# Performance work log

Measured on AMD Instinct MI355X. Metric: run time of the kernel, lower is better.

The kernel has to match this reference:

```python
import jax, jax.numpy as jnp
import numpy as np

N_NODES = 50000
N_EDGES = 800000
IN_CH = 128
EDGE_DIM = 32
H1, H2, H3, OUT = 128, 64, 32, 1


def _linear_params(key, fan_in, fan_out, bias=True):
    k1, k2 = jax.random.split(key)
    scale = 1.0 / np.sqrt(fan_in)
    W = jax.random.uniform(k1, (fan_in, fan_out), jnp.float32, -scale, scale)
    if bias:
        b = jax.random.uniform(k2, (fan_out,), jnp.float32, -scale, scale)
        return W, b
    return W


def setup_inputs() -> dict:
    key = jax.random.key(0)
    ks = jax.random.split(key, 32)
    inp = {
        'x': jax.random.normal(ks[0], (N_NODES, IN_CH), jnp.float32),
        'edge_index': jax.random.randint(ks[1], (2, N_EDGES), 0, N_NODES, jnp.int64),
        'edge_attr': jax.random.normal(ks[2], (N_EDGES, EDGE_DIM), jnp.float32),
    }
    dims = [(IN_CH, H1), (H1, H2), (H2, H3)]
    ki = 3
    for l, (fi, fo) in enumerate(dims, start=1):
        inp[f'Wq{l}'], inp[f'bq{l}'] = _linear_params(ks[ki], fi, fo); ki += 1
        inp[f'Wk{l}'], inp[f'bk{l}'] = _linear_params(ks[ki], fi, fo); ki += 1
        inp[f'Wv{l}'], inp[f'bv{l}'] = _linear_params(ks[ki], fi, fo); ki += 1
        inp[f'We{l}'] = _linear_params(ks[ki], EDGE_DIM, fo, bias=False); ki += 1
        inp[f'Ws{l}'], inp[f'bs{l}'] = _linear_params(ks[ki], fi, fo); ki += 1
    inp['Wc'], inp['bc'] = _linear_params(ks[ki], H3, OUT)
    return inp


def _tconv(x, src, dst, edge_attr, Wq, bq, Wk, bk, Wv, bv, We, Ws, bs):
    # TransformerConv, heads=1: edge-conditioned attention with segment softmax over dst
    q = x @ Wq + bq                      # [N, d]
    k = x @ Wk + bk                      # [N, d]
    v = x @ Wv + bv                      # [N, d]
    e = edge_attr @ We                   # [E, d]
    k_e = k[src] + e                     # gather + edge key
    v_e = v[src] + e                     # gather + edge value
    d = q.shape[-1]
    alpha = jnp.sum(q[dst] * k_e, axis=-1) / jnp.sqrt(jnp.asarray(d, x.dtype))  # [E]
    m = jax.ops.segment_max(alpha, dst, num_segments=N_NODES)
    a = jnp.exp(alpha - m[dst])
    s = jax.ops.segment_sum(a, dst, num_segments=N_NODES)
    a = a / s[dst]
    agg = jax.ops.segment_sum(a[:, None] * v_e, dst, num_segments=N_NODES)
    return agg + x @ Ws + bs             # root/skip connection


def reference(x, edge_index, edge_attr,
              Wq1, bq1, Wk1, bk1, Wv1, bv1, We1, Ws1, bs1,
              Wq2, bq2, Wk2, bk2, Wv2, bv2, We2, Ws2, bs2,
              Wq3, bq3, Wk3, bk3, Wv3, bv3, We3, Ws3, bs3,
              Wc, bc):
    src, dst = edge_index[0], edge_index[1]
    h = jax.nn.relu(_tconv(x, src, dst, edge_attr, Wq1, bq1, Wk1, bk1, Wv1, bv1, We1, Ws1, bs1))
    h = jax.nn.relu(_tconv(h, src, dst, edge_attr, Wq2, bq2, Wk2, bk2, Wv2, bv2, We2, Ws2, bs2))
    h = jax.nn.relu(_tconv(h, src, dst, edge_attr, Wq3, bq3, Wk3, bk3, Wv3, bv3, We3, Ws3, bs3))
    return h @ Wc + bc
```

## Files before the change

### kernel.cpp

```cpp
#include <hip/hip_runtime.h>
#include <math.h>

#define N_NODES 50000
#define N_EDGES 800000

typedef __bf16 bf16;
typedef __bf16 bf16x8 __attribute__((ext_vector_type(8)));
typedef float f32x4 __attribute__((ext_vector_type(4)));

__device__ __forceinline__ float bflo(unsigned r) {
  union { unsigned u; float f; } c; c.u = r << 16; return c.f;
}
__device__ __forceinline__ float bfhi(unsigned r) {
  union { unsigned u; float f; } c; c.u = r & 0xffff0000u; return c.f;
}

__device__ __forceinline__ float dot2bf(unsigned a, unsigned b, float acc) {
#if defined(__has_builtin)
#if __has_builtin(__builtin_amdgcn_fdot2_f32_bf16)
  typedef __bf16 bf16x2 __attribute__((ext_vector_type(2)));
  union { unsigned u; bf16x2 v; } ca, cb;
  ca.u = a; cb.u = b;
  return __builtin_amdgcn_fdot2_f32_bf16(ca.v, cb.v, acc, false);
#else
  return acc + bflo(a) * bflo(b) + bfhi(a) * bfhi(b);
#endif
#else
  return acc + bflo(a) * bflo(b) + bfhi(a) * bfhi(b);
#endif
}

__global__ void k_detect(const int* ei, int* flags) {
  if (threadIdx.x == 0 && blockIdx.x == 0) {
    int is64 = 1;
    for (int i = 0; i < 128; ++i) {
      if (ei[2 * i + 1] != 0) { is64 = 0; break; }
    }
    flags[0] = is64;
  }
}

__device__ __forceinline__ int load_idx(const int* ei, int e, int is64, int which) {
  size_t idx = (size_t)which * N_EDGES + (size_t)e;
  return is64 ? ei[2 * idx] : ei[idx];
}


__global__ void k_zero(int* p, int n) {
  int i = blockIdx.x * blockDim.x + threadIdx.x;
  if (i < n) p[i] = 0;
}

__global__ void k_hist(const int* ei, const int* flags, int* counts) {
  int e = blockIdx.x * blockDim.x + threadIdx.x;
  int is64 = flags[0];
  if (e < N_EDGES) {
    int dst = load_idx(ei, e, is64, 1);
    if (dst >= 0 && dst < N_NODES) atomicAdd(&counts[dst], 1);
  }
}

__global__ void k_scan1(const int* counts, int* row_ptr, int* bsum) {
  __shared__ int buf[1024];
  int t = threadIdx.x;
  int i = blockIdx.x * 1024 + t;
  int v = (i < N_NODES) ? counts[i] : 0;
  buf[t] = v;
  __syncthreads();
  for (int off = 1; off < 1024; off <<= 1) {
    int x = (t >= off) ? buf[t - off] : 0;
    __syncthreads();
    buf[t] += x;
    __syncthreads();
  }
  if (i < N_NODES) row_ptr[i] = buf[t] - v;
  if (t == 1023) bsum[blockIdx.x] = buf[1023];
}

__global__ void k_scan2(int* bsum, int* row_ptr) {
  constexpr int NB = (N_NODES + 1023) / 1024;
  int t = threadIdx.x;
  int v = (t < NB) ? bsum[t] : 0;
  int inc = v;
#pragma unroll
  for (int off = 1; off < 64; off <<= 1) {
    int x = __shfl_up(inc, off, 64);
    if (t >= off) inc += x;
  }
  if (t < NB) bsum[t] = inc - v;
  if (t == 63) row_ptr[N_NODES] = inc;
}

__global__ void k_scan3(const int* bsum, int* row_ptr, int* cursor) {
  int i = blockIdx.x * 1024 + threadIdx.x;
  if (i < N_NODES) {
    int r = row_ptr[i] + bsum[blockIdx.x];
    row_ptr[i] = r;
    cursor[i] = r;
  }
}

__global__ void k_scatter(const int* ei, const int* flags, int* cursor,
                          int* csr_src, int* csr_eid) {
  int e = blockIdx.x * blockDim.x + threadIdx.x;
  int is64 = flags[0];
  if (e < N_EDGES) {
    int src = load_idx(ei, e, is64, 0);
    int dst = load_idx(ei, e, is64, 1);
    if (dst >= 0 && dst < N_NODES && src >= 0 && src < N_NODES) {
      int pos = atomicAdd(&cursor[dst], 1);
      if (pos >= 0 && pos < N_EDGES) {
        csr_src[pos] = src;
        csr_eid[pos] = e;
      }
    }
  }
}


__global__ void k_eaperm(const float* __restrict__ ea, const int* __restrict__ csr_eid,
                         bf16* __restrict__ ea_bf) {
  int idx = blockIdx.x * blockDim.x + threadIdx.x;
  if (idx >= N_EDGES * 16) return;
  int p = idx >> 4, jj = idx & 15;
  int eid = csr_eid[p];
  float2 t = *(const float2*)(ea + (size_t)eid * 32 + 2 * jj);
  union { bf16 b[2]; unsigned u; } c;
  c.b[0] = (bf16)t.x; c.b[1] = (bf16)t.y;
  *(unsigned*)(ea_bf + (size_t)p * 32 + 2 * jj) = c.u;
}


#define DBLK 256
#define NDB ((N_NODES + DBLK - 1) / DBLK)

__global__ void k_dhist(const int* __restrict__ counts, int* __restrict__ btot) {
  __shared__ int lh[64];
  int t = threadIdx.x;
  if (t < 64) lh[t] = 0;
  __syncthreads();
  int n = blockIdx.x * DBLK + t;
  if (n < N_NODES) atomicAdd(&lh[min(counts[n], 63)], 1);
  __syncthreads();
  if (t < 64 && lh[t] > 0) atomicAdd(&btot[t], lh[t]);
}

__global__ void k_dbase(const int* __restrict__ btot, int* __restrict__ dcursor) {
  int t = threadIdx.x;
  int v = btot[t];
  int inc = v;
#pragma unroll
  for (int off = 1; off < 64; off <<= 1) {
    int x = __shfl_up(inc, off, 64);
    if (t >= off) inc += x;
  }
  dcursor[t] = inc - v;
}

__global__ void k_dscatter(const int* __restrict__ counts, int* __restrict__ dcursor,
                           int* __restrict__ node_perm) {
  __shared__ int lh[64];
  __shared__ int lbase[64];
  int t = threadIdx.x;
  if (t < 64) lh[t] = 0;
  __syncthreads();
  int n = blockIdx.x * DBLK + t;
  int b = 0, lrank = 0;
  bool valid = (n < N_NODES);
  if (valid) {
    b = min(counts[n], 63);
    lrank = atomicAdd(&lh[b], 1);
  }
  __syncthreads();
  if (t < 64) {
    int c = lh[t];
    lbase[t] = (c > 0) ? atomicAdd(&dcursor[t], c) : 0;
  }
  __syncthreads();
  if (valid) node_perm[lbase[b] + lrank] = n;
}


template <int FI, int FO>
__global__ void k_prep(const float* __restrict__ Wq, const float* __restrict__ bq,
                       const float* __restrict__ Wk, const float* __restrict__ bk,
                       const float* __restrict__ Wv, const float* __restrict__ bv,
                       const float* __restrict__ We,
                       const float* __restrict__ Ws, const float* __restrict__ bs,
                       bf16* __restrict__ Wt, float* __restrict__ bias) {
  constexpr int CPL = FO / 16;
  int n = blockIdx.x;
  int k = threadIdx.x;
  int pos;
  if (n < 4 * FO) {
    int sel = n / FO, c = n - sel * FO;
    if (sel == 0) pos = c;
    else if (sel == 3) pos = 3 * FO + c;
    else {
      int g = c / CPL, o = c - g * CPL;
      pos = FO + g * 2 * CPL + (sel == 2 ? CPL : 0) + o;
    }
  } else {
    pos = n;
  }
  if (n < 4 * FO) {
    int sel = n / FO, c = n - sel * FO;
    const float* W = sel == 0 ? Wq : sel == 1 ? Wk : sel == 2 ? Wv : Ws;
    Wt[(size_t)pos * FI + k] = (bf16)W[(size_t)k * FO + c];
    if (k == 0) bias[pos] = (sel == 0 ? bq : sel == 1 ? bk : sel == 2 ? bv : bs)[c];
  } else {
    int j = n - 4 * FO;
    float acc = 0.f;
    for (int c = 0; c < FO; ++c) acc += Wq[(size_t)k * FO + c] * We[(size_t)j * FO + c];
    Wt[(size_t)pos * FI + k] = (bf16)acc;
    if (k == 0) {
      float b = 0.f;
      for (int c = 0; c < FO; ++c) b += bq[c] * We[(size_t)j * FO + c];
      bias[pos] = b;
    }
  }
}


template <int K, int NT, bool AF32>
__global__ __launch_bounds__(256) void k_gemm_mfma(const void* __restrict__ A,
                                                   const bf16* __restrict__ Wt,
                                                   const float* __restrict__ bias,
                                                   bf16* __restrict__ feat) {
  constexpr int NKB = K / 32;
  constexpr int NCH = (NT + 63) / 64;
  int lane = threadIdx.x & 63;
  int wave = threadIdx.x >> 6;
  int m0 = blockIdx.x * 64 + wave * 16;
  if (m0 >= N_NODES) return;
  int half = lane & 15;
  int quad = lane >> 4;

  bf16x8 afr[NKB];
#pragma unroll
  for (int kb = 0; kb < NKB; ++kb) {
    size_t aoff = (size_t)(m0 + half) * K + kb * 32 + quad * 8;
    if constexpr (AF32) {
      const float* Af = (const float*)A;
      f32x4 lo = *(const f32x4*)(Af + aoff);
      f32x4 hi = *(const f32x4*)(Af + aoff + 4);
#pragma unroll
      for (int j = 0; j < 4; ++j) { afr[kb][j] = (bf16)lo[j]; afr[kb][4 + j] = (bf16)hi[j]; }
    } else {
      afr[kb] = *(const bf16x8*)((const bf16*)A + aoff);
    }
  }

  for (int ch = 0; ch < NCH; ++ch) {
    int c0 = ch * 64;
    f32x4 acc[4] = {};
#pragma unroll
    for (int kb = 0; kb < NKB; ++kb) {
#pragma unroll
      for (int f = 0; f < 4; ++f) {
        int cb = c0 + f * 16;
        if (cb < NT) {
          bf16x8 b = *(const bf16x8*)(Wt + (size_t)(cb + half) * K + kb * 32 + quad * 8);
          acc[f] = __builtin_amdgcn_mfma_f32_16x16x32_bf16(b, afr[kb], acc[f], 0, 0, 0);
        }
      }
    }
#pragma unroll
    for (int f = 0; f < 4; ++f) {
      int cb = c0 + f * 16;
      if (cb < NT) {
        int fcol = cb + quad * 4;
        f32x4 bv = *(const f32x4*)(bias + fcol);
        union { bf16 b[4]; uint2 u; } pk;
#pragma unroll
        for (int r = 0; r < 4; ++r) pk.b[r] = (bf16)(acc[f][r] + bv[r]);
        *(uint2*)(feat + (size_t)(m0 + half) * NT + fcol) = pk.u;
      }
    }
  }
}


template <int FO, bool FINAL, bool PERM>
__global__ __launch_bounds__(256) void k_edge(const bf16* __restrict__ feat,
                                              const float* __restrict__ ea,
                                              const bf16* __restrict__ ea_bf,
                                              const int* __restrict__ row_ptr,
                                              const int* __restrict__ csr_src,
                                              const int* __restrict__ csr_eid,
                                              const int* __restrict__ node_perm,
                                              const float* __restrict__ We,
                                              bf16* __restrict__ h_out,
                                              const float* __restrict__ Wc,
                                              const float* __restrict__ bc,
                                              float* __restrict__ out) {
  constexpr int FTOT = 4 * FO + 32;
  constexpr int CPL = FO / 16;
  constexpr int NU = CPL / 2;
  int lane16 = threadIdx.x & 15;
  int gid = blockIdx.x * 16 + (threadIdx.x >> 4);
  int node = node_perm[N_NODES - 1 - gid];
  int cbase = CPL * lane16;
  const bf16* fq = feat + (size_t)node * FTOT;

  unsigned qr[NU];
  {
    const unsigned* qp = (const unsigned*)(fq + cbase);
    if constexpr (NU == 4) { uint4 t = *(const uint4*)qp; qr[0]=t.x; qr[1]=t.y; qr[2]=t.z; qr[3]=t.w; }
    else if constexpr (NU == 2) { uint2 t = *(const uint2*)qp; qr[0]=t.x; qr[1]=t.y; }
    else { qr[0] = *qp; }
  }
  float qe0, qe1;
  { unsigned r = *(const unsigned*)(fq + 4 * FO + 2 * lane16); qe0 = bflo(r); qe1 = bfhi(r); }

  float m = -INFINITY, ssum = 0.f, wacc0 = 0.f, wacc1 = 0.f;
  float vacc[CPL];
#pragma unroll
  for (int i = 0; i < CPL; ++i) vacc[i] = 0.f;

  int start = row_ptr[node], end = row_ptr[node + 1];
  const float scaleA = 1.0f / sqrtf((float)FO);

  auto loadkv = [&](int src, unsigned* kv) {
    const unsigned* base = (const unsigned*)(feat + (size_t)src * FTOT + FO) + CPL * lane16;
    if constexpr (CPL == 8) {
      uint4 a = *(const uint4*)base; uint4 b = *(const uint4*)(base + 4);
      kv[0]=a.x; kv[1]=a.y; kv[2]=a.z; kv[3]=a.w; kv[4]=b.x; kv[5]=b.y; kv[6]=b.z; kv[7]=b.w;
    } else if constexpr (CPL == 4) {
      uint4 a = *(const uint4*)base;
      kv[0]=a.x; kv[1]=a.y; kv[2]=a.z; kv[3]=a.w;
    } else {
      uint2 a = *(const uint2*)base;
      kv[0]=a.x; kv[1]=a.y;
    }
  };

  auto loadea = [&](int p, float& e0, float& e1) {
    if constexpr (PERM) {
      unsigned r = *(const unsigned*)(ea_bf + (size_t)p * 32 + 2 * lane16);
      e0 = bflo(r); e1 = bfhi(r);
    } else {
      int eid = csr_eid[p];
      float2 t = *(const float2*)(ea + (size_t)eid * 32 + 2 * lane16);
      e0 = t.x; e1 = t.y;
    }
  };

  auto update = [&](const unsigned* kv, float e0, float e1) {
    float part = qe0 * e0 + qe1 * e1;
#pragma unroll
    for (int u = 0; u < NU; ++u) part = dot2bf(kv[u], qr[u], part);
#pragma unroll
    for (int off = 1; off < 16; off <<= 1) part += __shfl_xor(part, off, 64);
    float alpha = part * scaleA;
    float mnew = fmaxf(m, alpha);
    float sc = __expf(m - mnew);
    float w = __expf(alpha - mnew);
    ssum = ssum * sc + w;
#pragma unroll
    for (int u = 0; u < NU; ++u) {
      float a = bflo(kv[NU + u]), b = bfhi(kv[NU + u]);
      vacc[2*u]   = vacc[2*u]   * sc + w * a;
      vacc[2*u+1] = vacc[2*u+1] * sc + w * b;
    }
    wacc0 = wacc0 * sc + w * e0;
    wacc1 = wacc1 * sc + w * e1;
    m = mnew;
  };

  int p = start;
  for (; p + 4 <= end; p += 4) {
    int s[4];
#pragma unroll
    for (int u = 0; u < 4; ++u) s[u] = csr_src[p + u];
    unsigned kv[4][8];
#pragma unroll
    for (int u = 0; u < 4; ++u) loadkv(s[u], kv[u]);
    float e0[4], e1[4];
#pragma unroll
    for (int u = 0; u < 4; ++u) loadea(p + u, e0[u], e1[u]);
#pragma unroll
    for (int u = 0; u < 4; ++u) update(kv[u], e0[u], e1[u]);
  }
  for (; p < end; ++p) {
    unsigned kv0[8];
    loadkv(csr_src[p], kv0);
    float e0, e1;
    loadea(p, e0, e1);
    update(kv0, e0, e1);
  }

  float inv = (ssum > 0.f) ? 1.0f / ssum : 0.f;
  float agg[CPL];
#pragma unroll
  for (int i = 0; i < CPL; ++i) agg[i] = vacc[i];
#pragma unroll
  for (int jh = 0; jh < 16; ++jh) {
    float w0 = __shfl(wacc0, jh, 16);
    float w1 = __shfl(wacc1, jh, 16);
    const float* r0 = We + (size_t)(2 * jh) * FO + cbase;
    const float* r1 = We + (size_t)(2 * jh + 1) * FO + cbase;
#pragma unroll
    for (int i = 0; i < CPL; ++i) agg[i] += w0 * r0[i] + w1 * r1[i];
  }
  float hv[CPL];
#pragma unroll
  for (int i = 0; i < CPL; ++i) {
    float s = (float)fq[3 * FO + cbase + i];
    hv[i] = fmaxf(agg[i] * inv + s, 0.f);
  }
  if constexpr (!FINAL) {
    unsigned o[NU];
#pragma unroll
    for (int u = 0; u < NU; ++u) {
      union { bf16 b[2]; unsigned u32; } c;
      c.b[0] = (bf16)hv[2*u]; c.b[1] = (bf16)hv[2*u+1];
      o[u] = c.u32;
    }
    unsigned* dst = (unsigned*)(h_out + (size_t)node * FO + cbase);
    if constexpr (NU == 4) { uint4 t; t.x=o[0]; t.y=o[1]; t.z=o[2]; t.w=o[3]; *(uint4*)dst = t; }
    else if constexpr (NU == 2) { uint2 t; t.x=o[0]; t.y=o[1]; *(uint2*)dst = t; }
    else { *dst = o[0]; }
  } else {
    float part2 = 0.f;
#pragma unroll
    for (int i = 0; i < CPL; ++i) part2 += hv[i] * Wc[cbase + i];
#pragma unroll
    for (int off = 1; off < 16; off <<= 1) part2 += __shfl_xor(part2, off, 64);
    if (lane16 == 0) out[node] = part2 + bc[0];
  }
}


extern "C" void kernel_launch(void* const* d_in, const int* in_sizes, int n_in,
                              void* d_out, int out_size, void* d_ws, size_t ws_size,
                              hipStream_t stream) {
  (void)in_sizes; (void)n_in; (void)out_size;
  const float* x = (const float*)d_in[0];
  const int* ei = (const int*)d_in[1];
  const float* ea = (const float*)d_in[2];
  const float *Wq1 = (const float*)d_in[3], *bq1 = (const float*)d_in[4];
  const float *Wk1 = (const float*)d_in[5], *bk1 = (const float*)d_in[6];
  const float *Wv1 = (const float*)d_in[7], *bv1 = (const float*)d_in[8];
  const float *We1 = (const float*)d_in[9];
  const float *Ws1 = (const float*)d_in[10], *bs1 = (const float*)d_in[11];
  const float *Wq2 = (const float*)d_in[12], *bq2 = (const float*)d_in[13];
  const float *Wk2 = (const float*)d_in[14], *bk2 = (const float*)d_in[15];
  const float *Wv2 = (const float*)d_in[16], *bv2 = (const float*)d_in[17];
  const float *We2 = (const float*)d_in[18];
  const float *Ws2 = (const float*)d_in[19], *bs2 = (const float*)d_in[20];
  const float *Wq3 = (const float*)d_in[21], *bq3 = (const float*)d_in[22];
  const float *Wk3 = (const float*)d_in[23], *bk3 = (const float*)d_in[24];
  const float *Wv3 = (const float*)d_in[25], *bv3 = (const float*)d_in[26];
  const float *We3 = (const float*)d_in[27];
  const float *Ws3 = (const float*)d_in[28], *bs3 = (const float*)d_in[29];
  const float *Wc = (const float*)d_in[30], *bc = (const float*)d_in[31];

  char* ws = (char*)d_ws;
  size_t off = 0;
  auto alloc = [&](size_t bytes) -> void* {
    void* p = ws + off;
    off = (off + bytes + 255) & ~(size_t)255;
    return p;
  };
  bf16* h        = (bf16*)alloc((size_t)N_NODES * 128 * 2);
  int* counts    = (int*)alloc((N_NODES + 1) * 4);
  int* row_ptr   = (int*)alloc((N_NODES + 1) * 4);
  int* cursor    = (int*)alloc((N_NODES + 1) * 4);
  int* csr_src   = (int*)alloc((size_t)N_EDGES * 4);
  int* csr_eid   = (int*)alloc((size_t)N_EDGES * 4);
  int* flags     = (int*)alloc(256);
  bf16* Wt       = (bf16*)alloc(544 * 128 * 2);
  float* bias    = (float*)alloc(544 * 4);
  bf16* feat     = (bf16*)alloc((size_t)N_NODES * 544 * 2);
  int* bsum      = (int*)alloc(64 * 4);
  int* dcount    = (int*)alloc(64 * 4);
  int* dcursor   = (int*)alloc(64 * 4);
  int* node_perm = (int*)alloc((size_t)N_NODES * 4);
  bf16* ea_bf    = (bf16*)alloc((size_t)N_EDGES * 32 * 2);
  bool use_perm = (ws_size == 0) || (off <= ws_size);

  constexpr int NB = (N_NODES + 1023) / 1024;
  constexpr int GB = (N_NODES + 63) / 64;

  k_detect<<<1, 1, 0, stream>>>(ei, flags);
  k_zero<<<(N_NODES + 256) / 256, 256, 0, stream>>>(counts, N_NODES + 1);
  k_zero<<<1, 64, 0, stream>>>(dcount, 64);
  k_hist<<<(N_EDGES + 255) / 256, 256, 0, stream>>>(ei, flags, counts);
  k_scan1<<<NB, 1024, 0, stream>>>(counts, row_ptr, bsum);
  k_scan2<<<1, 64, 0, stream>>>(bsum, row_ptr);
  k_scan3<<<NB, 1024, 0, stream>>>(bsum, row_ptr, cursor);
  k_dhist<<<NDB, DBLK, 0, stream>>>(counts, dcount);
  k_dbase<<<1, 64, 0, stream>>>(dcount, dcursor);
  k_dscatter<<<NDB, DBLK, 0, stream>>>(counts, dcursor, node_perm);
  k_scatter<<<(N_EDGES + 255) / 256, 256, 0, stream>>>(ei, flags, cursor, csr_src, csr_eid);
  if (use_perm) {
    k_eaperm<<<(N_EDGES * 16 + 255) / 256, 256, 0, stream>>>(ea, csr_eid, ea_bf);
  }

  k_prep<128, 128><<<544, 128, 0, stream>>>(Wq1, bq1, Wk1, bk1, Wv1, bv1, We1, Ws1, bs1,
                                            Wt, bias);
  k_gemm_mfma<128, 544, true><<<GB, 256, 0, stream>>>(x, Wt, bias, feat);
  if (use_perm)
    k_edge<128, false, true><<<N_NODES / 16, 256, 0, stream>>>(feat, ea, ea_bf, row_ptr,
                                                               csr_src, csr_eid, node_perm,
                                                               We1, h, nullptr, nullptr,
                                                               nullptr);
  else
    k_edge<128, false, false><<<N_NODES / 16, 256, 0, stream>>>(feat, ea, ea_bf, row_ptr,
                                                                csr_src, csr_eid, node_perm,
                                                                We1, h, nullptr, nullptr,
                                                                nullptr);

  k_prep<128, 64><<<288, 128, 0, stream>>>(Wq2, bq2, Wk2, bk2, Wv2, bv2, We2, Ws2, bs2,
                                           Wt, bias);
  k_gemm_mfma<128, 288, false><<<GB, 256, 0, stream>>>(h, Wt, bias, feat);
  if (use_perm)
    k_edge<64, false, true><<<N_NODES / 16, 256, 0, stream>>>(feat, ea, ea_bf, row_ptr,
                                                              csr_src, csr_eid, node_perm,
                                                              We2, h, nullptr, nullptr,
                                                              nullptr);
  else
    k_edge<64, false, false><<<N_NODES / 16, 256, 0, stream>>>(feat, ea, ea_bf, row_ptr,
                                                               csr_src, csr_eid, node_perm,
                                                               We2, h, nullptr, nullptr,
                                                               nullptr);

  k_prep<64, 32><<<160, 64, 0, stream>>>(Wq3, bq3, Wk3, bk3, Wv3, bv3, We3, Ws3, bs3,
                                         Wt, bias);
  k_gemm_mfma<64, 160, false><<<GB, 256, 0, stream>>>(h, Wt, bias, feat);
  if (use_perm)
    k_edge<32, true, true><<<N_NODES / 16, 256, 0, stream>>>(feat, ea, ea_bf, row_ptr,
                                                             csr_src, csr_eid, node_perm,
                                                             We3, nullptr, Wc, bc,
                                                             (float*)d_out);
  else
    k_edge<32, true, false><<<N_NODES / 16, 256, 0, stream>>>(feat, ea, ea_bf, row_ptr,
                                                              csr_src, csr_eid, node_perm,
                                                              We3, nullptr, Wc, bc,
                                                              (float*)d_out);
}
```

Baseline: 654.0 us.

## Split GEMM column chunks across waves with shared 16-row A tile in LDS

Each block now handles 16 rows instead of 64. The 16-row A tile is staged once into padded shared memory, and the four waves split the 64-wide output column chunks among themselves, instead of each wave doing all columns for its own 16 rows. This cuts per-wave serial work and quadruples the grid, which adds parallelism and should help latency hiding. The cost is that the weight matrix is re-read by four times as many blocks. For NT=160 (3 chunks) one wave sits idle, and N_NODES/16 assumes exact divisibility.

Result: no change. 643.5 us (-1.6%).

```diff
diff --git a/kernel.cpp b/kernel.cpp
--- a/kernel.cpp
+++ b/kernel.cpp
@@ -229,29 +229,40 @@
                                                    bf16* __restrict__ feat) {
   constexpr int NKB = K / 32;
   constexpr int NCH = (NT + 63) / 64;
-  int lane = threadIdx.x & 63;
-  int wave = threadIdx.x >> 6;
-  int m0 = blockIdx.x * 64 + wave * 16;
-  if (m0 >= N_NODES) return;
+  constexpr int KP = K + 8;
+  __shared__ bf16 xs[16 * KP];
+  int t = threadIdx.x;
+  int lane = t & 63;
+  int wave = t >> 6;
+  int m0 = blockIdx.x * 16;
+
+  {
+    int base = t * 8;
+    if (base < 16 * K) {
+      int row = base / K, col = base - row * K;
+      union { bf16 b[8]; uint4 u; } pk;
+      if constexpr (AF32) {
+        const float* Af = (const float*)A + (size_t)(m0 + row) * K + col;
+        f32x4 lo = *(const f32x4*)Af;
+        f32x4 hi = *(const f32x4*)(Af + 4);
+#pragma unroll
+        for (int j = 0; j < 4; ++j) { pk.b[j] = (bf16)lo[j]; pk.b[4 + j] = (bf16)hi[j]; }
+      } else {
+        pk.u = *(const uint4*)((const bf16*)A + (size_t)(m0 + row) * K + col);
+      }
+      *(uint4*)(xs + row * KP + col) = pk.u;
+    }
+  }
+  __syncthreads();
+
   int half = lane & 15;
   int quad = lane >> 4;
-
   bf16x8 afr[NKB];
 #pragma unroll
-  for (int kb = 0; kb < NKB; ++kb) {
-    size_t aoff = (size_t)(m0 + half) * K + kb * 32 + quad * 8;
-    if constexpr (AF32) {
-      const float* Af = (const float*)A;
-      f32x4 lo = *(const f32x4*)(Af + aoff);
-      f32x4 hi = *(const f32x4*)(Af + aoff + 4);
-#pragma unroll
-      for (int j = 0; j < 4; ++j) { afr[kb][j] = (bf16)lo[j]; afr[kb][4 + j] = (bf16)hi[j]; }
-    } else {
-      afr[kb] = *(const bf16x8*)((const bf16*)A + aoff);
-    }
-  }
-
-  for (int ch = 0; ch < NCH; ++ch) {
+  for (int kb = 0; kb < NKB; ++kb)
+    afr[kb] = *(const bf16x8*)(xs + half * KP + kb * 32 + quad * 8);
+
+  for (int ch = wave; ch < NCH; ch += 4) {
     int c0 = ch * 64;
     f32x4 acc[4] = {};
 #pragma unroll
@@ -481,7 +492,7 @@
   bool use_perm = (ws_size == 0) || (off <= ws_size);
 
   constexpr int NB = (N_NODES + 1023) / 1024;
-  constexpr int GB = (N_NODES + 63) / 64;
+  constexpr int GB16 = N_NODES / 16;
 
   k_detect<<<1, 1, 0, stream>>>(ei, flags);
   k_zero<<<(N_NODES + 256) / 256, 256, 0, stream>>>(counts, N_NODES + 1);
@@ -500,7 +511,7 @@
 
   k_prep<128, 128><<<544, 128, 0, stream>>>(Wq1, bq1, Wk1, bk1, Wv1, bv1, We1, Ws1, bs1,
                                             Wt, bias);
-  k_gemm_mfma<128, 544, true><<<GB, 256, 0, stream>>>(x, Wt, bias, feat);
+  k_gemm_mfma<128, 544, true><<<GB16, 256, 0, stream>>>(x, Wt, bias, feat);
   if (use_perm)
     k_edge<128, false, true><<<N_NODES / 16, 256, 0, stream>>>(feat, ea, ea_bf, row_ptr,
                                                                csr_src, csr_eid, node_perm,
@@ -514,7 +525,7 @@
 
   k_prep<128, 64><<<288, 128, 0, stream>>>(Wq2, bq2, Wk2, bk2, Wv2, bv2, We2, Ws2, bs2,
                                            Wt, bias);
-  k_gemm_mfma<128, 288, false><<<GB, 256, 0, stream>>>(h, Wt, bias, feat);
+  k_gemm_mfma<128, 288, false><<<GB16, 256, 0, stream>>>(h, Wt, bias, feat);
   if (use_perm)
     k_edge<64, false, true><<<N_NODES / 16, 256, 0, stream>>>(feat, ea, ea_bf, row_ptr,
                                                               csr_src, csr_eid, node_perm,
@@ -528,7 +539,7 @@
 
   k_prep<64, 32><<<160, 64, 0, stream>>>(Wq3, bq3, Wk3, bk3, Wv3, bv3, We3, Ws3, bs3,
                                          Wt, bias);
-  k_gemm_mfma<64, 160, false><<<GB, 256, 0, stream>>>(h, Wt, bias, feat);
+  k_gemm_mfma<64, 160, false><<<GB16, 256, 0, stream>>>(h, Wt, bias, feat);
   if (use_perm)
     k_edge<32, true, true><<<N_NODES / 16, 256, 0, stream>>>(feat, ea, ea_bf, row_ptr,
                                                              csr_src, csr_eid, node_perm,
```

## Stage GEMM weight chunks into swizzled LDS with async double buffering

Applied to the files above, without the earlier changes.

The MFMA GEMM now copies each 64-column chunk of the transposed weight matrix into shared memory using global_load_lds, double-buffered so the next chunk loads while the current one is computed. k_prep writes the weights with an XOR swizzle so that LDS reads avoid bank conflicts. Previously every wave read its B fragments straight from global/L2. The change adds a block-wide barrier per chunk and 32-64KB of LDS per block, which may lower occupancy. Waves past the end of the node range stay in the loop so they still reach the barriers.

After: 576.4 us. -11.9%, faster.

```diff
diff --git a/kernel.cpp b/kernel.cpp
--- a/kernel.cpp
+++ b/kernel.cpp
@@ -28,6 +28,12 @@
 #else
   return acc + bflo(a) * bflo(b) + bfhi(a) * bfhi(b);
 #endif
+}
+
+__device__ __forceinline__ void gload_lds16(const void* g, void* l) {
+  __builtin_amdgcn_global_load_lds(
+      (const __attribute__((address_space(1))) void*)g,
+      (__attribute__((address_space(3))) void*)l, 16, 0, 0);
 }
 
 __global__ void k_detect(const int* ei, int* flags) {
@@ -203,16 +209,17 @@
   } else {
     pos = n;
   }
+  int ks = k ^ ((pos & 7) << 3);
   if (n < 4 * FO) {
     int sel = n / FO, c = n - sel * FO;
     const float* W = sel == 0 ? Wq : sel == 1 ? Wk : sel == 2 ? Wv : Ws;
-    Wt[(size_t)pos * FI + k] = (bf16)W[(size_t)k * FO + c];
+    Wt[(size_t)pos * FI + ks] = (bf16)W[(size_t)k * FO + c];
     if (k == 0) bias[pos] = (sel == 0 ? bq : sel == 1 ? bk : sel == 2 ? bv : bs)[c];
   } else {
     int j = n - 4 * FO;
     float acc = 0.f;
     for (int c = 0; c < FO; ++c) acc += Wq[(size_t)k * FO + c] * We[(size_t)j * FO + c];
-    Wt[(size_t)pos * FI + k] = (bf16)acc;
+    Wt[(size_t)pos * FI + ks] = (bf16)acc;
     if (k == 0) {
       float b = 0.f;
       for (int c = 0; c < FO; ++c) b += bq[c] * We[(size_t)j * FO + c];
@@ -229,54 +236,80 @@
                                                    bf16* __restrict__ feat) {
   constexpr int NKB = K / 32;
   constexpr int NCH = (NT + 63) / 64;
-  int lane = threadIdx.x & 63;
-  int wave = threadIdx.x >> 6;
-  int m0 = blockIdx.x * 64 + wave * 16;
-  if (m0 >= N_NODES) return;
+  constexpr int CHB = 64 * K * 2;
+  __shared__ char wbuf[2 * CHB];
+  int t = threadIdx.x;
+  int lane = t & 63;
+  int w = t >> 6;
   int half = lane & 15;
   int quad = lane >> 4;
+  int m0 = blockIdx.x * 64 + w * 16;
+  bool act = (m0 < N_NODES);
 
   bf16x8 afr[NKB];
-#pragma unroll
-  for (int kb = 0; kb < NKB; ++kb) {
-    size_t aoff = (size_t)(m0 + half) * K + kb * 32 + quad * 8;
-    if constexpr (AF32) {
-      const float* Af = (const float*)A;
-      f32x4 lo = *(const f32x4*)(Af + aoff);
-      f32x4 hi = *(const f32x4*)(Af + aoff + 4);
-#pragma unroll
-      for (int j = 0; j < 4; ++j) { afr[kb][j] = (bf16)lo[j]; afr[kb][4 + j] = (bf16)hi[j]; }
-    } else {
-      afr[kb] = *(const bf16x8*)((const bf16*)A + aoff);
-    }
-  }
+  {
+    int row = act ? (m0 + half) : (N_NODES - 16 + half);
+#pragma unroll
+    for (int kb = 0; kb < NKB; ++kb) {
+      size_t aoff = (size_t)row * K + kb * 32 + quad * 8;
+      if constexpr (AF32) {
+        const float* Af = (const float*)A;
+        f32x4 lo = *(const f32x4*)(Af + aoff);
+        f32x4 hi = *(const f32x4*)(Af + aoff + 4);
+#pragma unroll
+        for (int j = 0; j < 4; ++j) { afr[kb][j] = (bf16)lo[j]; afr[kb][4 + j] = (bf16)hi[j]; }
+      } else {
+        afr[kb] = *(const bf16x8*)((const bf16*)A + aoff);
+      }
+    }
+  }
+
+  auto stage = [&](int ch, int b) {
+    int cols = NT - ch * 64; if (cols > 64) cols = 64;
+    int nb = cols * K * 2;
+    const char* gsrc = (const char*)Wt + (size_t)ch * 64 * K * 2;
+    char* lbase = wbuf + b * CHB;
+    for (int off = w * 1024; off < nb; off += 4096)
+      gload_lds16(gsrc + off + lane * 16, lbase + off);
+  };
+
+  stage(0, 0);
+  __syncthreads();
 
   for (int ch = 0; ch < NCH; ++ch) {
+    if (ch + 1 < NCH) stage(ch + 1, (ch + 1) & 1);
+    const char* lb = wbuf + (ch & 1) * CHB;
     int c0 = ch * 64;
     f32x4 acc[4] = {};
 #pragma unroll
-    for (int kb = 0; kb < NKB; ++kb) {
+    for (int f = 0; f < 4; ++f) {
+      int cb = c0 + f * 16;
+      if (cb < NT) {
+        int lc = f * 16 + half;
+#pragma unroll
+        for (int kb = 0; kb < NKB; ++kb) {
+          int lin = kb * 64 + quad * 16;
+          int swz = lin ^ ((lc & 7) << 4);
+          bf16x8 b = *(const bf16x8*)(lb + lc * (K * 2) + swz);
+          acc[f] = __builtin_amdgcn_mfma_f32_16x16x32_bf16(b, afr[kb], acc[f], 0, 0, 0);
+        }
+      }
+    }
+    if (act) {
 #pragma unroll
       for (int f = 0; f < 4; ++f) {
         int cb = c0 + f * 16;
         if (cb < NT) {
-          bf16x8 b = *(const bf16x8*)(Wt + (size_t)(cb + half) * K + kb * 32 + quad * 8);
-          acc[f] = __builtin_amdgcn_mfma_f32_16x16x32_bf16(b, afr[kb], acc[f], 0, 0, 0);
+          int fcol = cb + quad * 4;
+          f32x4 bv = *(const f32x4*)(bias + fcol);
+          union { bf16 b[4]; uint2 u; } pk;
+#pragma unroll
+          for (int r = 0; r < 4; ++r) pk.b[r] = (bf16)(acc[f][r] + bv[r]);
+          *(uint2*)(feat + (size_t)(m0 + half) * NT + fcol) = pk.u;
         }
       }
     }
-#pragma unroll
-    for (int f = 0; f < 4; ++f) {
-      int cb = c0 + f * 16;
-      if (cb < NT) {
-        int fcol = cb + quad * 4;
-        f32x4 bv = *(const f32x4*)(bias + fcol);
-        union { bf16 b[4]; uint2 u; } pk;
-#pragma unroll
-        for (int r = 0; r < 4; ++r) pk.b[r] = (bf16)(acc[f][r] + bv[r]);
-        *(uint2*)(feat + (size_t)(m0 + half) * NT + fcol) = pk.u;
-      }
-    }
+    __syncthreads();
   }
 }
 
@@ -481,7 +514,7 @@
   bool use_perm = (ws_size == 0) || (off <= ws_size);
 
   constexpr int NB = (N_NODES + 1023) / 1024;
-  constexpr int GB = (N_NODES + 63) / 64;
+  constexpr int GB64 = (N_NODES + 63) / 64;
 
   k_detect<<<1, 1, 0, stream>>>(ei, flags);
   k_zero<<<(N_NODES + 256) / 256, 256, 0, stream>>>(counts, N_NODES + 1);
@@ -500,7 +533,7 @@
 
   k_prep<128, 128><<<544, 128, 0, stream>>>(Wq1, bq1, Wk1, bk1, Wv1, bv1, We1, Ws1, bs1,
                                             Wt, bias);
-  k_gemm_mfma<128, 544, true><<<GB, 256, 0, stream>>>(x, Wt, bias, feat);
+  k_gemm_mfma<128, 544, true><<<GB64, 256, 0, stream>>>(x, Wt, bias, feat);
   if (use_perm)
     k_edge<128, false, true><<<N_NODES / 16, 256, 0, stream>>>(feat, ea, ea_bf, row_ptr,
                                                                csr_src, csr_eid, node_perm,
@@ -514,7 +547,7 @@
 
   k_prep<128, 64><<<288, 128, 0, stream>>>(Wq2, bq2, Wk2, bk2, Wv2, bv2, We2, Ws2, bs2,
                                            Wt, bias);
-  k_gemm_mfma<128, 288, false><<<GB, 256, 0, stream>>>(h, Wt, bias, feat);
+  k_gemm_mfma<128, 288, false><<<GB64, 256, 0, stream>>>(h, Wt, bias, feat);
   if (use_perm)
     k_edge<64, false, true><<<N_NODES / 16, 256, 0, stream>>>(feat, ea, ea_bf, row_ptr,
                                                               csr_src, csr_eid, node_perm,
@@ -528,7 +561,7 @@
 
   k_prep<64, 32><<<160, 64, 0, stream>>>(Wq3, bq3, Wk3, bk3, Wv3, bv3, We3, Ws3, bs3,
                                          Wt, bias);
-  k_gemm_mfma<64, 160, false><<<GB, 256, 0, stream>>>(h, Wt, bias, feat);
+  k_gemm_mfma<64, 160, false><<<GB64, 256, 0, stream>>>(h, Wt, bias, feat);
   if (use_perm)
     k_edge<32, true, true><<<N_NODES / 16, 256, 0, stream>>>(feat, ea, ea_bf, row_ptr,
                                                              csr_src, csr_eid, node_perm,
```
